# Kernel optimization log

Measured on AMD Instinct MI355X. Metric: run time of the kernel, lower is better.

## Reference

```python
import jax, jax.numpy as jnp
import numpy as np

EPS = 1e-6

def setup_inputs() -> dict:
    key = jax.random.key(0)
    ks = jax.random.split(key, 5)
    B, C, H, W = 16, 512, 64, 64
    D = C // 8
    x = jax.random.normal(ks[0], (B, C, H, W), dtype=jnp.float32)
    Wq = jax.random.normal(ks[1], (D, C), dtype=jnp.float32) * (1.0 / np.sqrt(C))
    Wk = jax.random.normal(ks[2], (D, C), dtype=jnp.float32) * (1.0 / np.sqrt(C))
    Wv = jax.random.normal(ks[3], (C, C), dtype=jnp.float32) * (1.0 / np.sqrt(C))
    bq = jnp.zeros((D,), jnp.float32)
    bk = jnp.zeros((D,), jnp.float32)
    bv = jnp.zeros((C,), jnp.float32)
    gamma = jnp.ones((1,), jnp.float32)
    return {"x": x, "Wq": Wq, "bq": bq, "Wk": Wk, "bk": bk, "Wv": Wv, "bv": bv, "gamma": gamma}

def reference(x, Wq, bq, Wk, bk, Wv, bv, gamma):
    B, C, H, W = x.shape
    n = H * W
    xf = x.reshape(B, C, n)                                   # flatten spatial -> sequence
    # 1x1 convs == per-pixel linear projections
    Q = jnp.einsum('dc,bcn->bnd', Wq, xf) + bq                # (B, n, d)
    K = jnp.einsum('dc,bcn->bdn', Wk, xf) + bk[:, None]       # (B, d, n)
    V = jnp.einsum('dc,bcn->bdn', Wv, xf) + bv[:, None]       # (B, C, n)
    Q = jax.nn.softplus(Q)
    K = jax.nn.softplus(K)
    KV = jnp.einsum('bmn,bcn->bmc', K, V)                     # (B, d, C) linear-attention aggregation
    norm = 1.0 / jnp.einsum('bnm,bm->bn', Q, K.sum(-1) + EPS)  # (B, n)
    wv = jnp.einsum('bnm,bmc,bn->bcn', Q, KV, norm)           # (B, C, n)
    return (x + gamma[0] * wv.reshape(B, C, H, W))
```

## Files before the change

kernel.cpp:

```cpp
#include <hip/hip_runtime.h>
#include <hip/hip_bf16.h>
#include <math.h>

#define BB 16
#define CC 512
#define DD 64
#define NN 4096
#define EPSV 1e-6f
#define NCH 8

typedef __attribute__((ext_vector_type(8))) short short8;
typedef __attribute__((ext_vector_type(4))) short s16x4;
typedef __attribute__((ext_vector_type(4))) float f32x4;

__device__ __forceinline__ float softplus_f(float v) {
    return fmaxf(v, 0.0f) + __logf(1.0f + __expf(-fabsf(v)));
}
__device__ __forceinline__ short bf16s(float f) {
    __hip_bfloat16 h = __float2bfloat16(f);
    return __builtin_bit_cast(short, h);
}
__device__ __forceinline__ float sbf16(short s) {
    return __bfloat162float(__builtin_bit_cast(__hip_bfloat16, s));
}

__global__ __launch_bounds__(256) void k_prep(const float* __restrict__ Wq,
                                              const float* __restrict__ Wk,
                                              __hip_bfloat16* __restrict__ Wcat,
                                              float* __restrict__ Ksum) {
    int blk = blockIdx.x;
    if (blk < 256) {
        int i = blk * 256 + threadIdx.x;
        int j = i >> 9, c = i & 511;
        float v = (j < DD) ? Wq[j * CC + c] : Wk[(j - DD) * CC + c];
        Wcat[i] = __float2bfloat16(v);
    } else {
        f32x4 z = {0.f, 0.f, 0.f, 0.f};
        reinterpret_cast<f32x4*>(Ksum)[threadIdx.x] = z;
    }
}

__global__ __launch_bounds__(256) void k_proj(const float* __restrict__ x,
                                              const __hip_bfloat16* __restrict__ Wcat,
                                              const float* __restrict__ bq,
                                              const float* __restrict__ bk,
                                              __hip_bfloat16* __restrict__ Qb,
                                              __hip_bfloat16* __restrict__ Kb,
                                              float* __restrict__ Ksum) {
    __shared__ unsigned short xs[2][32][132];
    __shared__ unsigned short ws[2][128][40];

    int b = blockIdx.y;
    int n_blk = blockIdx.x * 128;
    int t = threadIdx.x;
    int wave = t >> 6, lane = t & 63;
    int nwl = wave * 32;
    int n_wave = n_blk + nwl;
    int l16 = lane & 15, g = lane >> 4;

    int sv = t & 31;
    int sc = t >> 5;
    int wj = t >> 1;
    int wh = t & 1;

    const float* xb = x + (size_t)b * CC * NN + n_blk + sv * 4;
    const unsigned short* wg = reinterpret_cast<const unsigned short*>(Wcat)
                               + (size_t)wj * 512 + wh * 16;

    f32x4 xr[4];
    s16x4 wr[4];

    auto loadx = [&](int c0) {
#pragma unroll
        for (int i = 0; i < 4; ++i)
            xr[i] = *reinterpret_cast<const f32x4*>(xb + (size_t)(c0 + sc + i * 8) * NN);
    };
    auto loadw = [&](int c0) {
#pragma unroll
        for (int k = 0; k < 4; ++k)
            wr[k] = *reinterpret_cast<const s16x4*>(wg + c0 + k * 4);
    };
    auto writex = [&](int bi) {
#pragma unroll
        for (int i = 0; i < 4; ++i) {
            s16x4 pv;
#pragma unroll
            for (int j = 0; j < 4; ++j) pv[j] = bf16s(xr[i][j]);
            *reinterpret_cast<s16x4*>(&xs[bi][sc + i * 8][sv * 4]) = pv;
        }
    };
    auto writew = [&](int bi) {
#pragma unroll
        for (int k = 0; k < 4; ++k)
            *reinterpret_cast<s16x4*>(&ws[bi][wj][wh * 16 + k * 4]) = wr[k];
    };

    f32x4 accQ[2][4] = {};
    f32x4 accK[4][2] = {};

    loadx(0); loadw(0);
    writex(0); writew(0);

    for (int ck = 0; ck < 16; ++ck) {
        int cur = ck & 1;
        if (ck < 15) { loadx((ck + 1) * 32); loadw((ck + 1) * 32); }
        asm volatile("s_waitcnt lgkmcnt(0)" ::: "memory");
        __builtin_amdgcn_s_barrier();
        short8 xf[2], wf[8];
#pragma unroll
        for (int nf = 0; nf < 2; ++nf) {
            short8 v;
#pragma unroll
            for (int e = 0; e < 8; ++e)
                v[e] = (short)xs[cur][g * 8 + e][nwl + nf * 16 + l16];
            xf[nf] = v;
        }
#pragma unroll
        for (int jf = 0; jf < 8; ++jf)
            wf[jf] = *reinterpret_cast<const short8*>(&ws[cur][jf * 16 + l16][g * 8]);
#pragma unroll
        for (int nf = 0; nf < 2; ++nf)
#pragma unroll
            for (int jf = 0; jf < 4; ++jf)
                accQ[nf][jf] = __builtin_amdgcn_mfma_f32_16x16x32_bf16(xf[nf], wf[jf], accQ[nf][jf], 0, 0, 0);
#pragma unroll
        for (int jf = 0; jf < 4; ++jf)
#pragma unroll
            for (int nf = 0; nf < 2; ++nf)
                accK[jf][nf] = __builtin_amdgcn_mfma_f32_16x16x32_bf16(wf[4 + jf], xf[nf], accK[jf][nf], 0, 0, 0);
        if (ck < 15) { writex(cur ^ 1); writew(cur ^ 1); }
    }

#pragma unroll
    for (int nf = 0; nf < 2; ++nf)
#pragma unroll
        for (int jf = 0; jf < 4; ++jf)
#pragma unroll
            for (int r = 0; r < 4; ++r) {
                int n = n_wave + nf * 16 + 4 * g + r;
                int j = jf * 16 + l16;
                float v = softplus_f(accQ[nf][jf][r] + bq[j]);
                Qb[((size_t)b * NN + n) * DD + j] = __float2bfloat16(v);
            }
#pragma unroll
    for (int jf = 0; jf < 4; ++jf)
#pragma unroll
        for (int r = 0; r < 4; ++r) {
            int m = jf * 16 + 4 * g + r;
            float s = 0.f;
#pragma unroll
            for (int nf = 0; nf < 2; ++nf) {
                int n = n_wave + nf * 16 + l16;
                float v = softplus_f(accK[jf][nf][r] + bk[m]);
                Kb[((size_t)b * DD + m) * NN + n] = __float2bfloat16(v);
                s += v;
            }
            s += __shfl_xor(s, 1, 64);
            s += __shfl_xor(s, 2, 64);
            s += __shfl_xor(s, 4, 64);
            s += __shfl_xor(s, 8, 64);
            if (l16 == 0) atomicAdd(&Ksum[b * DD + m], s);
        }
}

__global__ __launch_bounds__(256) void k_kx(const __hip_bfloat16* __restrict__ Kb,
                                            const float* __restrict__ x,
                                            float* __restrict__ KXp) {
    int b = blockIdx.z;
    int ch = blockIdx.y;
    int n0 = ch * 512;
    int c0 = blockIdx.x * 256;
    int wave = threadIdx.x >> 6, lane = threadIdx.x & 63;
    int cw = c0 + wave * 64;
    int l16 = lane & 15, g = lane >> 4;

    f32x4 acc[4][4] = {};
    const __hip_bfloat16* kp = Kb + (size_t)b * DD * NN;
    const float* xp = x + (size_t)b * CC * NN;

#pragma unroll 4
    for (int ks = 0; ks < 16; ++ks) {
        int nk = n0 + ks * 32 + g * 8;
        short8 af[4];
#pragma unroll
        for (int mi = 0; mi < 4; ++mi)
            af[mi] = *reinterpret_cast<const short8*>(kp + (size_t)(mi * 16 + l16) * NN + nk);
        short8 bf[4];
#pragma unroll
        for (int cj = 0; cj < 4; ++cj) {
            const float* xr = xp + (size_t)(cw + cj * 16 + l16) * NN + nk;
            f32x4 lo = *reinterpret_cast<const f32x4*>(xr);
            f32x4 hi = *reinterpret_cast<const f32x4*>(xr + 4);
            short8 v;
#pragma unroll
            for (int e = 0; e < 4; ++e) { v[e] = bf16s(lo[e]); v[4 + e] = bf16s(hi[e]); }
            bf[cj] = v;
        }
#pragma unroll
        for (int mi = 0; mi < 4; ++mi)
#pragma unroll
            for (int cj = 0; cj < 4; ++cj)
                acc[mi][cj] = __builtin_amdgcn_mfma_f32_16x16x32_bf16(af[mi], bf[cj], acc[mi][cj], 0, 0, 0);
    }
    float* kxd = KXp + (size_t)ch * BB * DD * CC + (size_t)b * DD * CC;
#pragma unroll
    for (int mi = 0; mi < 4; ++mi)
#pragma unroll
        for (int cj = 0; cj < 4; ++cj)
#pragma unroll
            for (int r = 0; r < 4; ++r) {
                int m = mi * 16 + 4 * g + r;
                int c = cw + cj * 16 + l16;
                kxd[(size_t)m * CC + c] = acc[mi][cj][r];
            }
}

__global__ __launch_bounds__(256) void k_red(const float* __restrict__ KXp,
                                             float* __restrict__ KX) {
    size_t i = (size_t)blockIdx.x * 256 + threadIdx.x;
    const f32x4* src = reinterpret_cast<const f32x4*>(KXp);
    size_t chstride = (size_t)BB * DD * CC / 4;
    f32x4 s = src[i];
#pragma unroll
    for (int ch = 1; ch < NCH; ++ch) {
        f32x4 v = src[ch * chstride + i];
        s[0] += v[0]; s[1] += v[1]; s[2] += v[2]; s[3] += v[3];
    }
    reinterpret_cast<f32x4*>(KX)[i] = s;
}

__global__ __launch_bounds__(256) void k_kv(const float* __restrict__ KX,
                                            const float* __restrict__ Wv,
                                            const float* __restrict__ bv,
                                            const float* __restrict__ Ksum,
                                            __hip_bfloat16* __restrict__ KVTb) {
    int b = blockIdx.y;
    int c0 = blockIdx.x * 64;
    int wave = threadIdx.x >> 6, lane = threadIdx.x & 63;
    int cw = c0 + wave * 16;
    int l16 = lane & 15, g = lane >> 4;

    f32x4 acc[4] = {};
    const float* wvp = Wv + (size_t)(cw + l16) * CC;
    const float* kxp = KX + (size_t)b * DD * CC;

#pragma unroll
    for (int ck = 0; ck < 16; ++ck) {
        int cp = ck * 32 + g * 8;
        f32x4 w0 = *reinterpret_cast<const f32x4*>(wvp + cp);
        f32x4 w1 = *reinterpret_cast<const f32x4*>(wvp + cp + 4);
        short8 a_hi, a_lo;
#pragma unroll
        for (int e = 0; e < 4; ++e) {
            a_hi[e] = bf16s(w0[e]);     a_lo[e] = bf16s(w0[e] - sbf16(a_hi[e]));
            a_hi[4 + e] = bf16s(w1[e]); a_lo[4 + e] = bf16s(w1[e] - sbf16(a_hi[4 + e]));
        }
#pragma unroll
        for (int mj = 0; mj < 4; ++mj) {
            const float* kr = kxp + (size_t)(mj * 16 + l16) * CC + cp;
            f32x4 k0 = *reinterpret_cast<const f32x4*>(kr);
            f32x4 k1 = *reinterpret_cast<const f32x4*>(kr + 4);
            short8 b_hi, b_lo;
#pragma unroll
            for (int e = 0; e < 4; ++e) {
                b_hi[e] = bf16s(k0[e]);     b_lo[e] = bf16s(k0[e] - sbf16(b_hi[e]));
                b_hi[4 + e] = bf16s(k1[e]); b_lo[4 + e] = bf16s(k1[e] - sbf16(b_hi[4 + e]));
            }
            acc[mj] = __builtin_amdgcn_mfma_f32_16x16x32_bf16(a_hi, b_hi, acc[mj], 0, 0, 0);
            acc[mj] = __builtin_amdgcn_mfma_f32_16x16x32_bf16(a_lo, b_hi, acc[mj], 0, 0, 0);
            acc[mj] = __builtin_amdgcn_mfma_f32_16x16x32_bf16(a_hi, b_lo, acc[mj], 0, 0, 0);
        }
    }
#pragma unroll
    for (int mj = 0; mj < 4; ++mj)
#pragma unroll
        for (int r = 0; r < 4; ++r) {
            int c = cw + 4 * g + r;
            int m = mj * 16 + l16;
            KVTb[((size_t)b * CC + c) * DD + m] =
                __float2bfloat16(acc[mj][r] + bv[c] * Ksum[b * DD + m]);
        }
}

__global__ __launch_bounds__(256) void k_out(const float* __restrict__ x,
                                             const __hip_bfloat16* __restrict__ Qb,
                                             const __hip_bfloat16* __restrict__ KVTb,
                                             const float* __restrict__ Ksum,
                                             const float* __restrict__ gamma,
                                             float* __restrict__ out) {
    int b = blockIdx.z;
    int c_blk = blockIdx.x * 128, n_blk = blockIdx.y * 128;
    int wave = threadIdx.x >> 6, lane = threadIdx.x & 63;
    int cw = c_blk + (wave >> 1) * 64, nw = n_blk + (wave & 1) * 64;
    int l16 = lane & 15, g = lane >> 4;

    float ksv[2][8];
#pragma unroll
    for (int ck = 0; ck < 2; ++ck)
#pragma unroll
        for (int e = 0; e < 8; ++e)
            ksv[ck][e] = Ksum[b * DD + (ck * 4 + g) * 8 + e] + EPSV;

    f32x4 acc[4][4] = {};
    float dot[4] = {0.f, 0.f, 0.f, 0.f};
    const short8* ap = reinterpret_cast<const short8*>(KVTb) + ((size_t)b * CC + cw) * 8;
    const short8* bp = reinterpret_cast<const short8*>(Qb) + ((size_t)b * NN + nw) * 8;
#pragma unroll
    for (int ck = 0; ck < 2; ++ck) {
        int ch = ck * 4 + g;
        short8 af[4], bf[4];
#pragma unroll
        for (int i = 0; i < 4; ++i) af[i] = ap[(size_t)(i * 16 + l16) * 8 + ch];
#pragma unroll
        for (int i = 0; i < 4; ++i) bf[i] = bp[(size_t)(i * 16 + l16) * 8 + ch];
#pragma unroll
        for (int j = 0; j < 4; ++j)
#pragma unroll
            for (int e = 0; e < 8; ++e)
                dot[j] = fmaf(sbf16(bf[j][e]), ksv[ck][e], dot[j]);
#pragma unroll
        for (int i = 0; i < 4; ++i)
#pragma unroll
            for (int j = 0; j < 4; ++j)
                acc[i][j] = __builtin_amdgcn_mfma_f32_16x16x32_bf16(af[i], bf[j], acc[i][j], 0, 0, 0);
    }
    float gm = gamma[0];
    float sc[4];
#pragma unroll
    for (int j = 0; j < 4; ++j) {
        float d = dot[j];
        d += __shfl_xor(d, 16, 64);
        d += __shfl_xor(d, 32, 64);
        sc[j] = gm / d;
    }
    const float* xb = x + (size_t)b * CC * NN;
    float* ob = out + (size_t)b * CC * NN;
#pragma unroll
    for (int i = 0; i < 4; ++i)
#pragma unroll
        for (int r = 0; r < 4; ++r) {
            int c = cw + i * 16 + 4 * g + r;
            size_t rowoff = (size_t)c * NN;
#pragma unroll
            for (int j = 0; j < 4; ++j) {
                int n = nw + j * 16 + l16;
                float xv = __builtin_nontemporal_load(&xb[rowoff + n]);
                __builtin_nontemporal_store(xv + sc[j] * acc[i][j][r], &ob[rowoff + n]);
            }
        }
}

extern "C" void kernel_launch(void* const* d_in, const int* in_sizes, int n_in,
                              void* d_out, int out_size, void* d_ws, size_t ws_size,
                              hipStream_t stream) {
    const float* x     = (const float*)d_in[0];
    const float* Wq    = (const float*)d_in[1];
    const float* bq    = (const float*)d_in[2];
    const float* Wk    = (const float*)d_in[3];
    const float* bk    = (const float*)d_in[4];
    const float* Wv    = (const float*)d_in[5];
    const float* bv    = (const float*)d_in[6];
    const float* gamma = (const float*)d_in[7];
    float* out = (float*)d_out;

    float* ws    = (float*)d_ws;
    float* KX    = ws;
    float* KXp   = KX + (size_t)BB * DD * CC;
    float* Ksum  = KXp + (size_t)NCH * BB * DD * CC;
    __hip_bfloat16* Qb   = (__hip_bfloat16*)(Ksum + BB * DD);
    __hip_bfloat16* Kb   = Qb + (size_t)BB * NN * DD;
    __hip_bfloat16* KVTb = Kb + (size_t)BB * DD * NN;
    __hip_bfloat16* Wcat = KVTb + (size_t)BB * CC * DD;

    k_prep<<<dim3(257), dim3(256), 0, stream>>>(Wq, Wk, Wcat, Ksum);
    k_proj<<<dim3(NN / 128, BB), dim3(256), 0, stream>>>(x, Wcat, bq, bk, Qb, Kb, Ksum);
    k_kx<<<dim3(2, NCH, BB), dim3(256), 0, stream>>>(Kb, x, KXp);
    k_red<<<dim3(BB * DD * CC / 4 / 256), dim3(256), 0, stream>>>(KXp, KX);
    k_kv<<<dim3(CC / 64, BB), dim3(256), 0, stream>>>(KX, Wv, bv, Ksum, KVTb);
    k_out<<<dim3(CC / 128, NN / 128, BB), dim3(256), 0, stream>>>(x, Qb, KVTb, Ksum, gamma, out);
}
```

Baseline: 179.4 us.

## Cache bf16 copy of x in projection kernel and reuse downstream

The projection kernel already converts x to bf16 for its matrix multiply, and it now also writes that bf16 copy to workspace. The K·X kernel and the output kernel then read the bf16 copy instead of the fp32 input, which cuts global read traffic and removes the per-element conversion in the K·X kernel. In exchange, k_proj takes on an extra write stream. The residual add in the output kernel now uses a bf16-rounded x, which lowers output precision and may break accuracy tolerances.

New measurement: 161.7 us. 9.9% less time.

```diff
diff --git a/kernel.cpp b/kernel.cpp
--- a/kernel.cpp
+++ b/kernel.cpp
@@ -46,6 +46,7 @@
                                               const float* __restrict__ bk,
                                               __hip_bfloat16* __restrict__ Qb,
                                               __hip_bfloat16* __restrict__ Kb,
+                                              __hip_bfloat16* __restrict__ xb16,
                                               float* __restrict__ Ksum) {
     __shared__ unsigned short xs[2][32][132];
     __shared__ unsigned short ws[2][128][40];
@@ -64,6 +65,8 @@
     int wh = t & 1;
 
     const float* xb = x + (size_t)b * CC * NN + n_blk + sv * 4;
+    unsigned short* xg = reinterpret_cast<unsigned short*>(xb16)
+                         + (size_t)b * CC * NN + n_blk + sv * 4;
     const unsigned short* wg = reinterpret_cast<const unsigned short*>(Wcat)
                                + (size_t)wj * 512 + wh * 16;
 
@@ -80,13 +83,14 @@
         for (int k = 0; k < 4; ++k)
             wr[k] = *reinterpret_cast<const s16x4*>(wg + c0 + k * 4);
     };
-    auto writex = [&](int bi) {
+    auto writex = [&](int bi, int c0) {
 #pragma unroll
         for (int i = 0; i < 4; ++i) {
             s16x4 pv;
 #pragma unroll
             for (int j = 0; j < 4; ++j) pv[j] = bf16s(xr[i][j]);
             *reinterpret_cast<s16x4*>(&xs[bi][sc + i * 8][sv * 4]) = pv;
+            *reinterpret_cast<s16x4*>(&xg[(size_t)(c0 + sc + i * 8) * NN]) = pv;
         }
     };
     auto writew = [&](int bi) {
@@ -99,7 +103,7 @@
     f32x4 accK[4][2] = {};
 
     loadx(0); loadw(0);
-    writex(0); writew(0);
+    writex(0, 0); writew(0);
 
     for (int ck = 0; ck < 16; ++ck) {
         int cur = ck & 1;
@@ -128,7 +132,7 @@
 #pragma unroll
             for (int nf = 0; nf < 2; ++nf)
                 accK[jf][nf] = __builtin_amdgcn_mfma_f32_16x16x32_bf16(wf[4 + jf], xf[nf], accK[jf][nf], 0, 0, 0);
-        if (ck < 15) { writex(cur ^ 1); writew(cur ^ 1); }
+        if (ck < 15) { writex(cur ^ 1, (ck + 1) * 32); writew(cur ^ 1); }
     }
 
 #pragma unroll
@@ -164,7 +168,7 @@
 }
 
 __global__ __launch_bounds__(256) void k_kx(const __hip_bfloat16* __restrict__ Kb,
-                                            const float* __restrict__ x,
+                                            const __hip_bfloat16* __restrict__ xb16,
                                             float* __restrict__ KXp) {
     int b = blockIdx.z;
     int ch = blockIdx.y;
@@ -176,26 +180,18 @@
 
     f32x4 acc[4][4] = {};
     const __hip_bfloat16* kp = Kb + (size_t)b * DD * NN;
-    const float* xp = x + (size_t)b * CC * NN;
+    const __hip_bfloat16* xp = xb16 + (size_t)b * CC * NN;
 
 #pragma unroll 4
     for (int ks = 0; ks < 16; ++ks) {
         int nk = n0 + ks * 32 + g * 8;
-        short8 af[4];
+        short8 af[4], bf[4];
 #pragma unroll
         for (int mi = 0; mi < 4; ++mi)
             af[mi] = *reinterpret_cast<const short8*>(kp + (size_t)(mi * 16 + l16) * NN + nk);
-        short8 bf[4];
-#pragma unroll
-        for (int cj = 0; cj < 4; ++cj) {
-            const float* xr = xp + (size_t)(cw + cj * 16 + l16) * NN + nk;
-            f32x4 lo = *reinterpret_cast<const f32x4*>(xr);
-            f32x4 hi = *reinterpret_cast<const f32x4*>(xr + 4);
-            short8 v;
-#pragma unroll
-            for (int e = 0; e < 4; ++e) { v[e] = bf16s(lo[e]); v[4 + e] = bf16s(hi[e]); }
-            bf[cj] = v;
-        }
+#pragma unroll
+        for (int cj = 0; cj < 4; ++cj)
+            bf[cj] = *reinterpret_cast<const short8*>(xp + (size_t)(cw + cj * 16 + l16) * NN + nk);
 #pragma unroll
         for (int mi = 0; mi < 4; ++mi)
 #pragma unroll
@@ -282,7 +278,7 @@
         }
 }
 
-__global__ __launch_bounds__(256) void k_out(const float* __restrict__ x,
+__global__ __launch_bounds__(256) void k_out(const __hip_bfloat16* __restrict__ xb16,
                                              const __hip_bfloat16* __restrict__ Qb,
                                              const __hip_bfloat16* __restrict__ KVTb,
                                              const float* __restrict__ Ksum,
@@ -333,7 +329,7 @@
         d += __shfl_xor(d, 32, 64);
         sc[j] = gm / d;
     }
-    const float* xb = x + (size_t)b * CC * NN;
+    const __hip_bfloat16* xb = xb16 + (size_t)b * CC * NN;
     float* ob = out + (size_t)b * CC * NN;
 #pragma unroll
     for (int i = 0; i < 4; ++i)
@@ -344,7 +340,7 @@
 #pragma unroll
             for (int j = 0; j < 4; ++j) {
                 int n = nw + j * 16 + l16;
-                float xv = __builtin_nontemporal_load(&xb[rowoff + n]);
+                float xv = __bfloat162float(xb[rowoff + n]);
                 __builtin_nontemporal_store(xv + sc[j] * acc[i][j][r], &ob[rowoff + n]);
             }
         }
@@ -371,11 +367,12 @@
     __hip_bfloat16* Kb   = Qb + (size_t)BB * NN * DD;
     __hip_bfloat16* KVTb = Kb + (size_t)BB * DD * NN;
     __hip_bfloat16* Wcat = KVTb + (size_t)BB * CC * DD;
+    __hip_bfloat16* xb16 = Wcat + 128 * CC;
 
     k_prep<<<dim3(257), dim3(256), 0, stream>>>(Wq, Wk, Wcat, Ksum);
-    k_proj<<<dim3(NN / 128, BB), dim3(256), 0, stream>>>(x, Wcat, bq, bk, Qb, Kb, Ksum);
-    k_kx<<<dim3(2, NCH, BB), dim3(256), 0, stream>>>(Kb, x, KXp);
+    k_proj<<<dim3(NN / 128, BB), dim3(256), 0, stream>>>(x, Wcat, bq, bk, Qb, Kb, xb16, Ksum);
+    k_kx<<<dim3(2, NCH, BB), dim3(256), 0, stream>>>(Kb, xb16, KXp);
     k_red<<<dim3(BB * DD * CC / 4 / 256), dim3(256), 0, stream>>>(KXp, KX);
     k_kv<<<dim3(CC / 64, BB), dim3(256), 0, stream>>>(KX, Wv, bv, Ksum, KVTb);
-    k_out<<<dim3(CC / 128, NN / 128, BB), dim3(256), 0, stream>>>(x, Qb, KVTb, Ksum, gamma, out);
-}
+    k_out<<<dim3(CC / 128, NN / 128, BB), dim3(256), 0, stream>>>(xb16, Qb, KVTb, Ksum, gamma, out);
+}
```
